# Kernel tuning notes

Measured on AMD Instinct MI355X. Metric: run time of the kernel, lower is better.

The kernel has to match this reference:

```python
import jax, jax.numpy as jnp
import numpy as np

B, T, E, H, L, V = 16, 512, 512, 8, 4, 2048
HS = E // H  # head_size = n_embd // n_head
FF = 4 * E


def _ln(x, g, b):
    m = x.mean(-1, keepdims=True)
    v = ((x - m) ** 2).mean(-1, keepdims=True)
    return (x - m) * jax.lax.rsqrt(v + 1e-5) * g + b


def setup_inputs() -> dict:
    key = jax.random.key(0)
    ks = jax.random.split(key, 16)
    s = jnp.float32(0.02)
    return {
        "idx": jax.random.randint(ks[0], (B, T), 0, V),
        "tok_emb": jax.random.normal(ks[1], (V, E), jnp.float32) * s,
        "pos_emb": jax.random.normal(ks[2], (T, E), jnp.float32) * s,
        "Wq": jax.random.normal(ks[3], (L, E, E), jnp.float32) * s,
        "Wk": jax.random.normal(ks[4], (L, E, E), jnp.float32) * s,
        "Wv": jax.random.normal(ks[5], (L, E, E), jnp.float32) * s,
        "rel": jax.random.normal(ks[6], (L, 2 * T - 1, HS), jnp.float32) * s,
        "Wo": jax.random.normal(ks[7], (L, E, E), jnp.float32) * s,
        "bo": jnp.zeros((L, E), jnp.float32),
        "ln1_g": jnp.ones((L, E), jnp.float32),
        "ln1_b": jnp.zeros((L, E), jnp.float32),
        "W1": jax.random.normal(ks[8], (L, E, FF), jnp.float32) * s,
        "b1": jnp.zeros((L, FF), jnp.float32),
        "W2": jax.random.normal(ks[9], (L, FF, E), jnp.float32) * s,
        "b2": jnp.zeros((L, E), jnp.float32),
        "ln2_g": jnp.ones((L, E), jnp.float32),
        "ln2_b": jnp.zeros((L, E), jnp.float32),
        "lnf_g": jnp.ones((E,), jnp.float32),
        "lnf_b": jnp.zeros((E,), jnp.float32),
        "Wlm": jax.random.normal(ks[10], (E, V), jnp.float32) * s,
        "blm": jnp.zeros((V,), jnp.float32),
    }


def reference(idx, tok_emb, pos_emb, Wq, Wk, Wv, rel, Wo, bo, ln1_g, ln1_b,
              W1, b1, W2, b2, ln2_g, ln2_b, lnf_g, lnf_b, Wlm, blm):
    x = tok_emb[idx] + pos_emb[None, :T]  # (B,T,E)
    ri = jnp.arange(T)
    rel_idx = ri[:, None] - ri[None, :] + (T - 1)  # block_size == T
    causal = ri[:, None] >= ri[None, :]            # (T,T) lower-triangular
    scale = jnp.float32(1.0 / np.sqrt(HS))
    for l in range(L):
        h = _ln(x, ln1_g[l], ln1_b[l])
        # NOTE: torch code does .view(B, H, T, HS) on a (B, T, H*HS) tensor
        # (NOT a transpose) -- jnp.reshape matches row-major view semantics.
        q = (h @ Wq[l]).reshape(B, H, T, HS)
        k = (h @ Wk[l]).reshape(B, H, T, HS)
        v = (h @ Wv[l]).reshape(B, H, T, HS)
        re = rel[l][rel_idx]  # (T,T,HS)
        # rel scores: sum_d q[b,h,i,d]*re[i,j,d]; avoid the 5D intermediate
        scores = jnp.einsum('bhid,bhjd->bhij', q, k) * scale \
               + jnp.einsum('bhid,ijd->bhij', q, re)
        scores = jnp.where(causal, scores, -jnp.inf)
        att = jax.nn.softmax(scores, axis=-1)  # dropout disabled (eval)
        ctx = jnp.einsum('bhij,bhjd->bhid', att, v)
        ctx = jnp.swapaxes(ctx, 1, 2).reshape(B, T, H * HS)
        x = x + ctx @ Wo[l] + bo[l]
        h2 = _ln(x, ln2_g[l], ln2_b[l])
        x = x + jax.nn.relu(h2 @ W1[l] + b1[l]) @ W2[l] + b2[l]
    x = _ln(x, lnf_g, lnf_b)
    return x @ Wlm + blm  # logits (B,T,V)
```

## Files before the change

### kernel.cpp

```cpp
#include <hip/hip_runtime.h>
#include <hip/hip_bf16.h>
#include <stdint.h>

typedef __hip_bfloat16 bf16;
typedef __attribute__((ext_vector_type(8))) short bf16x8;
typedef __attribute__((ext_vector_type(8))) short short8;
typedef __attribute__((ext_vector_type(4))) float f32x4;

#define DEV __device__ __forceinline__

static constexpr int Bn = 16, Tn = 512, En = 512, Hn = 8, Ln = 4, Vn = 2048;
static constexpr int HSn = 64, FFn = 2048, Mn = Bn * Tn;
static constexpr int SQ = 1536;

DEV f32x4 mfma16(bf16x8 a, bf16x8 b, f32x4 c) {
  return __builtin_amdgcn_mfma_f32_16x16x32_bf16(a, b, c, 0, 0, 0);
}
DEV float b2f(bf16 x) { return __bfloat162float(x); }
DEV bf16 f2b(float x) { return __float2bfloat16(x); }
DEV short f2s(float x) { bf16 h = f2b(x); return reinterpret_cast<short&>(h); }
DEV float s2f(short x) { return __bfloat162float(reinterpret_cast<bf16&>(x)); }

DEV void gload16(const void* g, void* l) {
  __builtin_amdgcn_global_load_lds(
      (const __attribute__((address_space(1))) void*)(uintptr_t)g,
      (__attribute__((address_space(3))) void*)(uint32_t)(uintptr_t)l, 16, 0, 0);
}

__global__ __launch_bounds__(256) void ktranspose(const float* __restrict__ in,
                                                  bf16* __restrict__ out, int R, int C,
                                                  long in_zs, long out_zs) {
  __shared__ float tile[32][33];
  int z = blockIdx.z;
  const float* inz = in + (size_t)z * in_zs;
  bf16* outz = out + (size_t)z * out_zs;
  int c0 = blockIdx.x * 32, r0 = blockIdx.y * 32;
  for (int k = 0; k < 32; k += 8)
    tile[threadIdx.y + k][threadIdx.x] =
        inz[(size_t)(r0 + threadIdx.y + k) * C + (c0 + threadIdx.x)];
  __syncthreads();
  for (int k = 0; k < 32; k += 8)
    outz[(size_t)(c0 + threadIdx.y + k) * R + (r0 + threadIdx.x)] =
        f2b(tile[threadIdx.x][threadIdx.y + k]);
}

__global__ __launch_bounds__(256) void kcast(const float* __restrict__ in,
                                             bf16* __restrict__ out, int n) {
  int i = blockIdx.x * 256 + threadIdx.x;
  if (i < n) out[i] = f2b(in[i]);
}

__global__ __launch_bounds__(256) void kembed(const int* __restrict__ idx,
                                              const float* __restrict__ tok,
                                              const float* __restrict__ pos,
                                              bf16* __restrict__ x) {
  int i = blockIdx.x * 256 + threadIdx.x;
  int e8 = (i & 63) * 8;
  int bt = i >> 6;
  int t = bt & (Tn - 1);
  const float* tp = tok + (size_t)idx[bt] * En + e8;
  const float* pp = pos + (size_t)t * En + e8;
  f32x4 t0 = *(const f32x4*)tp, t1 = *(const f32x4*)(tp + 4);
  f32x4 p0 = *(const f32x4*)pp, p1 = *(const f32x4*)(pp + 4);
  short8 ov;
  for (int j = 0; j < 4; j++) {
    ov[j] = f2s(t0[j] + p0[j]);
    ov[j + 4] = f2s(t1[j] + p1[j]);
  }
  *(short8*)(x + (size_t)bt * En + e8) = ov;
}

__global__ __launch_bounds__(256) void kln(const bf16* __restrict__ x,
                                           const float* __restrict__ g,
                                           const float* __restrict__ b,
                                           bf16* __restrict__ out) {
  int row = blockIdx.x * 4 + (threadIdx.x >> 6);
  int lane = threadIdx.x & 63;
  short8 xv = *(const short8*)(x + (size_t)row * En + lane * 8);
  float v[8], s = 0.f;
  for (int j = 0; j < 8; j++) { v[j] = s2f(xv[j]); s += v[j]; }
  for (int m = 1; m < 64; m <<= 1) s += __shfl_xor(s, m);
  float mean = s * (1.f / En);
  float s2 = 0.f;
  for (int j = 0; j < 8; j++) { float d = v[j] - mean; s2 += d * d; }
  for (int m = 1; m < 64; m <<= 1) s2 += __shfl_xor(s2, m);
  float rstd = rsqrtf(s2 * (1.f / En) + 1e-5f);
  f32x4 g0 = *(const f32x4*)(g + lane * 8), g1 = *(const f32x4*)(g + lane * 8 + 4);
  f32x4 b0 = *(const f32x4*)(b + lane * 8), b1 = *(const f32x4*)(b + lane * 8 + 4);
  short8 ov;
  for (int j = 0; j < 4; j++) {
    ov[j] = f2s((v[j] - mean) * rstd * g0[j] + b0[j]);
    ov[j + 4] = f2s((v[j + 4] - mean) * rstd * g1[j] + b1[j]);
  }
  *(short8*)(out + (size_t)row * En + lane * 8) = ov;
}

template <int BM, int BN, int TW, int DB, int SWZ, int NBIAS, int RELU, int MODE>
__global__ __launch_bounds__(TW) void kgemm(const bf16* __restrict__ A,
                                            const bf16* __restrict__ Bt,
                                            const float* __restrict__ bias,
                                            float* __restrict__ outf,
                                            bf16* __restrict__ outh, int Ndim, int K) {
  constexpr int NW = TW / 64;
  constexpr int WCN = NW / 2;
  constexpr int WM = BM / 2, WN = BN / WCN, MI = WM / 16, NI = WN / 16;
  constexpr int NB = DB ? 2 : 1;
  __shared__ bf16 As[NB][BM * 64];
  __shared__ bf16 Bs[NB][BN * 64];
  int t = threadIdx.x, lane = t & 63, w = t >> 6;
  int lr = lane & 15, lg = lane >> 4;
  int sx = lr & 7;
  int wr = w / WCN, wc = w % WCN;
  int bx, by;
  if (SWZ) {
    int id = blockIdx.x + gridDim.x * blockIdx.y;
    int xcd = id & 7, s = id >> 3;
    int gx = gridDim.x;
    by = xcd * 8 + s / gx;
    bx = s % gx;
  } else {
    bx = blockIdx.x; by = blockIdx.y;
  }
  int br = by * BM, bc = bx * BN;
  f32x4 acc[MI][NI] = {};
  int rl = lane >> 3, cb = (lane & 7) ^ rl;
  const bf16* Abase = A + (size_t)(br + w * (BM / NW) + rl) * K + cb * 8;
  const bf16* Bbase = Bt + (size_t)(bc + w * (BN / NW) + rl) * K + cb * 8;

  auto STAGE = [&](int buf, int kt) {
    for (int c = 0; c < BM / (8 * NW); c++)
      gload16(Abase + (size_t)(c * 8) * K + kt, &As[buf][(w * (BM / NW) + c * 8) * 64]);
    for (int c = 0; c < BN / (8 * NW); c++)
      gload16(Bbase + (size_t)(c * 8) * K + kt, &Bs[buf][(w * (BN / NW) + c * 8) * 64]);
  };
  auto COMPUTE = [&](int buf) {
    for (int kk = 0; kk < 2; kk++) {
      int gb = (kk * 4 + lg) ^ sx;
      bf16x8 af[MI], bfr[NI];
      for (int mi = 0; mi < MI; mi++)
        af[mi] = *(const bf16x8*)&As[buf][(wr * WM + mi * 16 + lr) * 64 + gb * 8];
      for (int ni = 0; ni < NI; ni++)
        bfr[ni] = *(const bf16x8*)&Bs[buf][(wc * WN + ni * 16 + lr) * 64 + gb * 8];
      for (int mi = 0; mi < MI; mi++)
        for (int ni = 0; ni < NI; ni++)
          acc[mi][ni] = mfma16(af[mi], bfr[ni], acc[mi][ni]);
    }
  };

  if (DB) {
    STAGE(0, 0);
    __syncthreads();
    int nt = K / 64;
    for (int t2 = 0; t2 < nt; t2++) {
      int cur = t2 & 1;
      if (t2 + 1 < nt) STAGE(cur ^ 1, (t2 + 1) * 64);
      COMPUTE(cur);
      __syncthreads();
    }
  } else {
    for (int kt = 0; kt < K; kt += 64) {
      __syncthreads();
      STAGE(0, kt);
      __syncthreads();
      COMPUTE(0);
    }
  }

  for (int mi = 0; mi < MI; mi++)
    for (int ni = 0; ni < NI; ni++)
      for (int r = 0; r < 4; r++) {
        int row = br + wr * WM + mi * 16 + lg * 4 + r;
        int col = bc + wc * WN + ni * 16 + lr;
        float val = acc[mi][ni][r];
        if (NBIAS) val += bias[col];
        if (RELU) val = fmaxf(val, 0.f);
        if (MODE == 1) {
          bf16* p = outh + (size_t)row * Ndim + col;
          *p = f2b(b2f(*p) + val);
        } else if (MODE == 2) {
          outf[(size_t)row * Ndim + col] = val;
        } else {
          outh[(size_t)row * Ndim + col] = f2b(val);
        }
      }
}

template <int NBIAS, int RELU, int MODE>
__global__ __launch_bounds__(512) void kgemm8(const bf16* __restrict__ A,
                                              const bf16* __restrict__ Bt,
                                              const float* __restrict__ bias,
                                              float* __restrict__ outf,
                                              bf16* __restrict__ outh, int Ndim, int K) {
  __shared__ bf16 As[2][256 * 64];
  __shared__ bf16 Bs[2][256 * 64];
  int t = threadIdx.x, lane = t & 63, w = t >> 6;
  int lr = lane & 15, lg = lane >> 4;
  int sx = lr & 7;
  int wr = w >> 2, wc = w & 3;
  int rl8 = lane >> 3, cb = (lane & 7) ^ rl8;
  int id = blockIdx.x + gridDim.x * blockIdx.y;
  int xcd = id & 7, s = id >> 3;
  int by = xcd * 4 + (s >> 3), bx = s & 7;
  int br = by * 256, bc = bx * 256;
  f32x4 acc[8][4] = {};
  const bf16* Abase = A + (size_t)(br + w * 16 + rl8) * K + cb * 8;
  const bf16* Bbase = Bt + (size_t)(bc + w * 16 + rl8) * K + cb * 8;

  auto STAGEH = [&](int hh, int buf, int kt) {
    int half = hh & 1;
    if (hh < 2) {
      const bf16* g = Abase + (size_t)(half * 128) * K + kt;
      bf16* l = &As[buf][(half * 128 + w * 16) * 64];
      gload16(g, l);
      gload16(g + (size_t)8 * K, l + 8 * 64);
    } else {
      const bf16* g = Bbase + (size_t)(half * 128) * K + kt;
      bf16* l = &Bs[buf][(half * 128 + w * 16) * 64];
      gload16(g, l);
      gload16(g + (size_t)8 * K, l + 8 * 64);
    }
  };

#define PHASE8(Q, P)                                                          \
  do {                                                                        \
    constexpr int mh = (Q) >> 1, nh = (Q) & 1;                                \
    bf16x8 af[4][2], bfr[2][2];                                               \
    _Pragma("unroll") for (int kk = 0; kk < 2; kk++) {                        \
      int gb = (kk * 4 + lg) ^ sx;                                            \
      _Pragma("unroll") for (int i = 0; i < 4; i++)                           \
        af[i][kk] = *(const bf16x8*)&As[P][(wr * 128 + (mh * 4 + i) * 16 + lr) * 64 + gb * 8]; \
      _Pragma("unroll") for (int j = 0; j < 2; j++)                           \
        bfr[j][kk] = *(const bf16x8*)&Bs[P][(wc * 64 + (nh * 2 + j) * 16 + lr) * 64 + gb * 8]; \
    }                                                                         \
    __builtin_amdgcn_s_setprio(1);                                            \
    _Pragma("unroll") for (int i = 0; i < 4; i++)                             \
      _Pragma("unroll") for (int j = 0; j < 2; j++) {                         \
        acc[mh * 4 + i][nh * 2 + j] =                                         \
            mfma16(af[i][0], bfr[j][0], acc[mh * 4 + i][nh * 2 + j]);         \
        acc[mh * 4 + i][nh * 2 + j] =                                         \
            mfma16(af[i][1], bfr[j][1], acc[mh * 4 + i][nh * 2 + j]);         \
      }                                                                       \
    __builtin_amdgcn_s_setprio(0);                                            \
  } while (0)

  int nt = K / 64;
  for (int hh = 0; hh < 4; hh++) STAGEH(hh, 0, 0);
  STAGEH(0, 1, 64);
  STAGEH(1, 1, 64);
  asm volatile("s_waitcnt vmcnt(4)" ::: "memory");
  asm volatile("s_barrier" ::: "memory");
  for (int t2 = 0; t2 < nt; t2++) {
    int p = t2 & 1;
    if (t2 + 1 < nt) STAGEH(2, p ^ 1, (t2 + 1) * 64);
    PHASE8(0, p);
    if (t2 + 1 < nt) STAGEH(3, p ^ 1, (t2 + 1) * 64);
    PHASE8(1, p);
    PHASE8(2, p);
    PHASE8(3, p);
    asm volatile("s_barrier" ::: "memory");
    if (t2 + 2 < nt) {
      STAGEH(0, p, (t2 + 2) * 64);
      STAGEH(1, p, (t2 + 2) * 64);
      asm volatile("s_waitcnt vmcnt(4)" ::: "memory");
      asm volatile("s_barrier" ::: "memory");
    } else if (t2 + 1 < nt) {
      asm volatile("s_waitcnt vmcnt(0)" ::: "memory");
      asm volatile("s_barrier" ::: "memory");
    }
  }
#undef PHASE8
#pragma unroll
  for (int mi = 0; mi < 8; mi++)
#pragma unroll
    for (int ni = 0; ni < 4; ni++)
#pragma unroll
      for (int r = 0; r < 4; r++) {
        int row = br + wr * 128 + mi * 16 + lg * 4 + r;
        int col = bc + wc * 64 + ni * 16 + lr;
        float val = acc[mi][ni][r];
        if (NBIAS) val += bias[col];
        if (RELU) val = fmaxf(val, 0.f);
        if (MODE == 2) outf[(size_t)row * Ndim + col] = val;
        else outh[(size_t)row * Ndim + col] = f2b(val);
      }
}

__global__ __launch_bounds__(512) void kattn(const bf16* __restrict__ qkv,
                                             const bf16* __restrict__ rel,
                                             bf16* __restrict__ ctx) {
  __shared__ bf16 Ks[128 * 64];
  __shared__ bf16 Vs[64 * 128];
  __shared__ bf16 Prel[8][16 * 81];
  __shared__ bf16 Ps[8][16 * 64];
  int pairp = blockIdx.x, bh = blockIdx.y;
  int b = bh >> 3, hh = bh & 7;
  int t = threadIdx.x, lane = t & 63, w = t >> 6;
  int wl = w & 3, wg = w >> 2;
  int lr = lane & 15, lg = lane >> 4;
  int sx = lr & 7;
  int rl8 = lane >> 3, cbk = (lane & 7) ^ rl8;
  const size_t headrow = (size_t)(b * Tn + hh * 64);
  bf16* prw = &Prel[w][0];
  bf16* psw = &Ps[w][0];
  int jp = t >> 3, db = (t & 7) * 8;

  int ia = pairp, ib = 7 - pairp;
  int myblk = wg ? ia : ib;
  int mylast = myblk * 64;
  int i0w = myblk * 64 + wl * 16;
  bf16x8 aq[2];
  {
    int t2 = i0w + lr;
    const bf16* qp = qkv + (headrow + (t2 >> 3)) * SQ + (t2 & 7) * 64;
    aq[0] = *(const bf16x8*)(qp + lg * 8);
    aq[1] = *(const bf16x8*)(qp + 32 + lg * 8);
  }
  f32x4 o[4] = {};
  float m_run = -3e38f, l_run = 0.f;
  int ntiles = (ib >> 1) + 1;

  auto SUBTILE = [&](int jb, bool diag, int su) {
    int njmax = diag ? wl : 3;
    int nmmin = diag ? 3 - wl : 0;
    __builtin_amdgcn_s_setprio(1);
    f32x4 sqk[4] = {};
    for (int nj = 0; nj <= njmax; nj++) {
      int row = su * 64 + nj * 16 + lr;
      bf16x8 kb0 = *(const bf16x8*)&Ks[row * 64 + ((lg ^ sx) * 8)];
      bf16x8 kb1 = *(const bf16x8*)&Ks[row * 64 + (((4 + lg) ^ sx) * 8)];
      sqk[nj] = mfma16(kb0, aq[0], sqk[nj]);
      sqk[nj] = mfma16(kb1, aq[1], sqk[nj]);
    }
    int base = i0w - jb + 448;
    for (int nm = nmmin; nm < 5; nm++) {
      int mrow = base + nm * 16 + lr;
      if (mrow > 1022) mrow = 1022;
      const bf16* rp = rel + (size_t)mrow * 64;
      f32x4 sr = {};
      sr = mfma16(aq[0], *(const bf16x8*)(rp + lg * 8), sr);
      sr = mfma16(aq[1], *(const bf16x8*)(rp + 32 + lg * 8), sr);
      for (int r = 0; r < 4; r++)
        prw[(lg * 4 + r) * 81 + nm * 16 + lr] = f2b(sr[r]);
    }
    __builtin_amdgcn_s_setprio(0);
    float sv[4][4];
    for (int nj = 0; nj < 4; nj++)
      for (int r = 0; r < 4; r++) sv[nj][r] = -3e38f;
    float mloc = -3e38f;
    for (int nj = 0; nj <= njmax; nj++)
      for (int r = 0; r < 4; r++) {
        int jj = nj * 16 + lg * 4 + r;
        float val = sqk[nj][r] * 0.125f + b2f(prw[lr * 81 + (lr - jj + 63)]);
        if (jb + jj > i0w + lr) val = -3e38f;
        sv[nj][r] = val;
        mloc = fmaxf(mloc, val);
      }
    mloc = fmaxf(mloc, __shfl_xor(mloc, 16));
    mloc = fmaxf(mloc, __shfl_xor(mloc, 32));
    float mnew = fmaxf(m_run, mloc);
    float corr = __expf(m_run - mnew);
    m_run = mnew;
    float lsum = 0.f;
    for (int nj = 0; nj < 4; nj++)
      for (int r = 0; r < 4; r++) {
        float p = __expf(sv[nj][r] - mnew);
        lsum += p;
        psw[lr * 64 + (((nj * 2 + (lg >> 1)) ^ sx) * 8) + (lg & 1) * 4 + r] = f2b(p);
      }
    lsum += __shfl_xor(lsum, 16);
    lsum += __shfl_xor(lsum, 32);
    l_run = l_run * corr + lsum;
    for (int r = 0; r < 4; r++) {
      float c = __shfl(corr, lg * 4 + r);
      for (int nd = 0; nd < 4; nd++) o[nd][r] *= c;
    }
    __builtin_amdgcn_s_setprio(1);
    bf16x8 ap0 = *(const bf16x8*)&psw[lr * 64 + ((lg ^ sx) * 8)];
    bf16x8 ap1 = *(const bf16x8*)&psw[lr * 64 + (((4 + lg) ^ sx) * 8)];
    for (int nd = 0; nd < 4; nd++) {
      int d = nd * 16 + lr;
      bf16x8 vb0 = *(const bf16x8*)&Vs[d * 128 + ((su * 8 + (lg ^ sx)) * 8)];
      bf16x8 vb1 = *(const bf16x8*)&Vs[d * 128 + ((su * 8 + ((4 + lg) ^ sx)) * 8)];
      o[nd] = mfma16(ap0, vb0, o[nd]);
      o[nd] = mfma16(ap1, vb1, o[nd]);
    }
    __builtin_amdgcn_s_setprio(0);
  };

  for (int jt = 0; jt < ntiles; jt++) {
    int jbase = jt * 128;
    bf16x8 vv[2];
#pragma unroll
    for (int u = 0; u < 2; u++) {
      int j0 = jbase + jp * 2 + u;
      vv[u] = *(const bf16x8*)(qkv + (headrow + (j0 >> 3)) * SQ + (j0 & 7) * 64 + 1024 + db);
    }
    __syncthreads();
#pragma unroll
    for (int c = 0; c < 2; c++) {
      int row = w * 16 + c * 8 + rl8;
      const bf16* src = qkv + (headrow + ((jbase + row) >> 3)) * SQ +
                        (row & 7) * 64 + 512 + cbk * 8;
      gload16(src, &Ks[(w * 16 + c * 8) * 64]);
    }
    {
      const short* pa = (const short*)&vv[0];
      const short* pb = (const short*)&vv[1];
      int j0 = jp * 2;
      int jblk = j0 >> 3, jin = j0 & 7;
#pragma unroll
      for (int u = 0; u < 8; u++) {
        int d = db + u;
        int idx = d * 128 + ((jblk ^ (d & 7)) * 8) + jin;
        uint32_t pk = (uint32_t)(uint16_t)pa[u] | ((uint32_t)(uint16_t)pb[u] << 16);
        *(uint32_t*)((short*)Vs + idx) = pk;
      }
    }
    __syncthreads();
#pragma unroll
    for (int su = 0; su < 2; su++) {
      int jb = jbase + su * 64;
      if (jb > ib * 64) break;
      if (jb <= mylast) SUBTILE(jb, jb == mylast, su);
    }
  }
  for (int r = 0; r < 4; r++) {
    float linv = 1.f / __shfl(l_run, lg * 4 + r);
    int row = i0w + lg * 4 + r;
    for (int nd = 0; nd < 4; nd++)
      ctx[((size_t)b * Tn + row) * En + hh * 64 + nd * 16 + lr] = f2b(o[nd][r] * linv);
  }
}

extern "C" void kernel_launch(void* const* d_in, const int* in_sizes, int n_in,
                              void* d_out, int out_size, void* d_ws, size_t ws_size,
                              hipStream_t stream) {
  (void)in_sizes; (void)n_in; (void)out_size; (void)ws_size;
  const int* idx = (const int*)d_in[0];
  const float* tok = (const float*)d_in[1];
  const float* pos = (const float*)d_in[2];
  const float* Wq = (const float*)d_in[3];
  const float* Wk = (const float*)d_in[4];
  const float* Wv = (const float*)d_in[5];
  const float* rel = (const float*)d_in[6];
  const float* Wo = (const float*)d_in[7];
  const float* bo = (const float*)d_in[8];
  const float* ln1_g = (const float*)d_in[9];
  const float* ln1_b = (const float*)d_in[10];
  const float* W1 = (const float*)d_in[11];
  const float* b1 = (const float*)d_in[12];
  const float* W2 = (const float*)d_in[13];
  const float* b2 = (const float*)d_in[14];
  const float* ln2_g = (const float*)d_in[15];
  const float* ln2_b = (const float*)d_in[16];
  const float* lnf_g = (const float*)d_in[17];
  const float* lnf_b = (const float*)d_in[18];
  const float* Wlm = (const float*)d_in[19];
  const float* blm = (const float*)d_in[20];

  char* ws = (char*)d_ws;
  bf16* x = (bf16*)(ws + 0);
  bf16* h = (bf16*)(ws + 16777216);
  bf16* qkv = (bf16*)(ws + 25165824);
  bf16* ctx = (bf16*)(ws + 50331648);
  bf16* ffn1 = qkv;
  bf16* wqkvT = (bf16*)(ws + 58720256);
  bf16* woT = wqkvT + (size_t)Ln * SQ * En;
  bf16* w1T = woT + (size_t)Ln * En * En;
  bf16* w2T = w1T + (size_t)Ln * En * FFn;
  bf16* wlmT = w2T + (size_t)Ln * FFn * En;
  bf16* relc = wlmT + (size_t)En * Vn;
  float* outf = (float*)d_out;

  dim3 tb(32, 8);
  ktranspose<<<dim3(16, 16, Ln), tb, 0, stream>>>(Wq, wqkvT, En, En, (long)En * En, (long)SQ * En);
  ktranspose<<<dim3(16, 16, Ln), tb, 0, stream>>>(Wk, wqkvT + 512 * 512, En, En, (long)En * En, (long)SQ * En);
  ktranspose<<<dim3(16, 16, Ln), tb, 0, stream>>>(Wv, wqkvT + 2 * 512 * 512, En, En, (long)En * En, (long)SQ * En);
  ktranspose<<<dim3(16, 16, Ln), tb, 0, stream>>>(Wo, woT, En, En, (long)En * En, (long)En * En);
  ktranspose<<<dim3(64, 16, Ln), tb, 0, stream>>>(W1, w1T, En, FFn, (long)En * FFn, (long)En * FFn);
  ktranspose<<<dim3(16, 64, Ln), tb, 0, stream>>>(W2, w2T, FFn, En, (long)FFn * En, (long)FFn * En);
  ktranspose<<<dim3(64, 16, 1), tb, 0, stream>>>(Wlm, wlmT, En, Vn, 0, 0);
  kcast<<<(Ln * (2 * Tn - 1) * HSn + 255) / 256, 256, 0, stream>>>(
      rel, relc, Ln * (2 * Tn - 1) * HSn);

  kembed<<<(Mn * En / 8) / 256, 256, 0, stream>>>(idx, tok, pos, x);

  for (int l = 0; l < Ln; l++) {
    kln<<<Mn / 4, 256, 0, stream>>>(x, ln1_g + (size_t)l * En, ln1_b + (size_t)l * En, h);
    kgemm<128, 128, 256, 0, 1, 0, 0, 0><<<dim3(12, 64), 256, 0, stream>>>(
        h, wqkvT + (size_t)l * SQ * En, nullptr, nullptr, qkv, SQ, En);
    kattn<<<dim3(4, 128), 512, 0, stream>>>(
        qkv, relc + (size_t)l * (2 * Tn - 1) * HSn, ctx);
    kgemm<128, 128, 512, 1, 1, 1, 0, 1><<<dim3(4, 64), 512, 0, stream>>>(
        ctx, woT + (size_t)l * En * En, bo + (size_t)l * En, nullptr, x, En, En);
    kln<<<Mn / 4, 256, 0, stream>>>(x, ln2_g + (size_t)l * En, ln2_b + (size_t)l * En, h);
    kgemm8<1, 1, 0><<<dim3(8, 32), 512, 0, stream>>>(
        h, w1T + (size_t)l * En * FFn, b1 + (size_t)l * FFn, nullptr, ffn1, FFn, En);
    kgemm<128, 128, 512, 1, 1, 1, 0, 1><<<dim3(4, 64), 512, 0, stream>>>(
        ffn1, w2T + (size_t)l * FFn * En, b2 + (size_t)l * En, nullptr, x, En, FFn);
  }
  kln<<<Mn / 4, 256, 0, stream>>>(x, lnf_g, lnf_b, h);
  kgemm8<1, 0, 2><<<dim3(8, 32), 512, 0, stream>>>(
      h, wlmT, blm, outf, nullptr, Vn, En);
}
```

Before: 611.5 us.

## Merge prep kernels into one launch and use 256x64 kgemm8 for N=512 GEMMs

Fuses the seven weight-transpose launches, the rel cast and the embedding into one kprep kernel that dispatches on block id, removing several launch gaps. Templates kgemm8 on the B-tile width and adds a 256x64 variant with residual-add output, then uses it for the Wo and W2 projections in place of the 128x128 kgemm. The new variant uses a lighter B staging path and a different pipeline schedule. It trades A-tile reuse per block for a different grid shape of 256 blocks with 8-way XCD-aware mapping.

```diff
diff --git a/kernel.cpp b/kernel.cpp
--- a/kernel.cpp
+++ b/kernel.cpp
@@ -27,47 +27,87 @@
       (__attribute__((address_space(3))) void*)(uint32_t)(uintptr_t)l, 16, 0, 0);
 }
 
-__global__ __launch_bounds__(256) void ktranspose(const float* __restrict__ in,
-                                                  bf16* __restrict__ out, int R, int C,
-                                                  long in_zs, long out_zs) {
-  __shared__ float tile[32][33];
-  int z = blockIdx.z;
-  const float* inz = in + (size_t)z * in_zs;
-  bf16* outz = out + (size_t)z * out_zs;
-  int c0 = blockIdx.x * 32, r0 = blockIdx.y * 32;
-  for (int k = 0; k < 32; k += 8)
-    tile[threadIdx.y + k][threadIdx.x] =
-        inz[(size_t)(r0 + threadIdx.y + k) * C + (c0 + threadIdx.x)];
-  __syncthreads();
-  for (int k = 0; k < 32; k += 8)
-    outz[(size_t)(c0 + threadIdx.y + k) * R + (r0 + threadIdx.x)] =
-        f2b(tile[threadIdx.x][threadIdx.y + k]);
-}
-
-__global__ __launch_bounds__(256) void kcast(const float* __restrict__ in,
-                                             bf16* __restrict__ out, int n) {
-  int i = blockIdx.x * 256 + threadIdx.x;
-  if (i < n) out[i] = f2b(in[i]);
-}
-
-__global__ __launch_bounds__(256) void kembed(const int* __restrict__ idx,
-                                              const float* __restrict__ tok,
-                                              const float* __restrict__ pos,
-                                              bf16* __restrict__ x) {
-  int i = blockIdx.x * 256 + threadIdx.x;
-  int e8 = (i & 63) * 8;
-  int bt = i >> 6;
-  int t = bt & (Tn - 1);
-  const float* tp = tok + (size_t)idx[bt] * En + e8;
-  const float* pp = pos + (size_t)t * En + e8;
-  f32x4 t0 = *(const f32x4*)tp, t1 = *(const f32x4*)(tp + 4);
-  f32x4 p0 = *(const f32x4*)pp, p1 = *(const f32x4*)(pp + 4);
-  short8 ov;
-  for (int j = 0; j < 4; j++) {
-    ov[j] = f2s(t0[j] + p0[j]);
-    ov[j + 4] = f2s(t1[j] + p1[j]);
-  }
-  *(short8*)(x + (size_t)bt * En + e8) = ov;
+__global__ __launch_bounds__(256) void kprep(
+    const float* __restrict__ Wq, const float* __restrict__ Wk,
+    const float* __restrict__ Wv, const float* __restrict__ Wo,
+    const float* __restrict__ W1, const float* __restrict__ W2,
+    const float* __restrict__ Wlm, const float* __restrict__ rel,
+    const int* __restrict__ idx, const float* __restrict__ tok,
+    const float* __restrict__ pos,
+    bf16* __restrict__ wqkvT, bf16* __restrict__ woT, bf16* __restrict__ w1T,
+    bf16* __restrict__ w2T, bf16* __restrict__ wlmT, bf16* __restrict__ relc,
+    bf16* __restrict__ x) {
+  int id = blockIdx.x;
+  if (id < 13312) {
+    const float* in;
+    bf16* out;
+    int R, C, z, cx, cy;
+    long in_zs, out_zs;
+    if (id < 3072) {
+      int part = id >> 10, inner = id & 1023;
+      z = inner >> 8;
+      int tile = inner & 255;
+      cx = tile & 15; cy = tile >> 4;
+      in = part == 0 ? Wq : (part == 1 ? Wk : Wv);
+      out = wqkvT + part * 512 * 512;
+      R = En; C = En; in_zs = (long)En * En; out_zs = (long)SQ * En;
+    } else if (id < 4096) {
+      int inner = id - 3072;
+      z = inner >> 8;
+      int tile = inner & 255;
+      cx = tile & 15; cy = tile >> 4;
+      in = Wo; out = woT; R = En; C = En;
+      in_zs = (long)En * En; out_zs = (long)En * En;
+    } else if (id < 8192) {
+      int inner = id - 4096;
+      z = inner >> 10;
+      int tile = inner & 1023;
+      cx = tile & 63; cy = tile >> 6;
+      in = W1; out = w1T; R = En; C = FFn;
+      in_zs = (long)En * FFn; out_zs = (long)En * FFn;
+    } else if (id < 12288) {
+      int inner = id - 8192;
+      z = inner >> 10;
+      int tile = inner & 1023;
+      cx = tile & 15; cy = tile >> 4;
+      in = W2; out = w2T; R = FFn; C = En;
+      in_zs = (long)FFn * En; out_zs = (long)FFn * En;
+    } else {
+      int tile = id - 12288;
+      z = 0;
+      cx = tile & 63; cy = tile >> 6;
+      in = Wlm; out = wlmT; R = En; C = Vn;
+      in_zs = 0; out_zs = 0;
+    }
+    __shared__ float tile_s[32][33];
+    int tx = threadIdx.x & 31, ty = threadIdx.x >> 5;
+    const float* inz = in + (size_t)z * in_zs;
+    bf16* outz = out + (size_t)z * out_zs;
+    int c0 = cx * 32, r0 = cy * 32;
+    for (int k = 0; k < 32; k += 8)
+      tile_s[ty + k][tx] = inz[(size_t)(r0 + ty + k) * C + (c0 + tx)];
+    __syncthreads();
+    for (int k = 0; k < 32; k += 8)
+      outz[(size_t)(c0 + ty + k) * R + (r0 + tx)] = f2b(tile_s[tx][ty + k]);
+  } else if (id < 14335) {
+    int i = (id - 13312) * 256 + threadIdx.x;
+    relc[i] = f2b(rel[i]);
+  } else {
+    int i = (id - 14335) * 256 + threadIdx.x;
+    int e8 = (i & 63) * 8;
+    int bt = i >> 6;
+    int t = bt & (Tn - 1);
+    const float* tp = tok + (size_t)idx[bt] * En + e8;
+    const float* pp = pos + (size_t)t * En + e8;
+    f32x4 t0 = *(const f32x4*)tp, t1 = *(const f32x4*)(tp + 4);
+    f32x4 p0 = *(const f32x4*)pp, p1 = *(const f32x4*)(pp + 4);
+    short8 ov;
+    for (int j = 0; j < 4; j++) {
+      ov[j] = f2s(t0[j] + p0[j]);
+      ov[j + 4] = f2s(t1[j] + p1[j]);
+    }
+    *(short8*)(x + (size_t)bt * En + e8) = ov;
+  }
 }
 
 __global__ __launch_bounds__(256) void kln(const bf16* __restrict__ x,
@@ -185,14 +225,16 @@
       }
 }
 
-template <int NBIAS, int RELU, int MODE>
+template <int BN, int NBIAS, int RELU, int MODE>
 __global__ __launch_bounds__(512) void kgemm8(const bf16* __restrict__ A,
                                               const bf16* __restrict__ Bt,
                                               const float* __restrict__ bias,
                                               float* __restrict__ outf,
                                               bf16* __restrict__ outh, int Ndim, int K) {
+  constexpr int NI = BN / 64;
+  constexpr int BROW = (BN == 256) ? 16 : 8;
   __shared__ bf16 As[2][256 * 64];
-  __shared__ bf16 Bs[2][256 * 64];
+  __shared__ bf16 Bs[2][BN * 64];
   int t = threadIdx.x, lane = t & 63, w = t >> 6;
   int lr = lane & 15, lg = lane >> 4;
   int sx = lr & 7;
@@ -201,87 +243,117 @@
   int id = blockIdx.x + gridDim.x * blockIdx.y;
   int xcd = id & 7, s = id >> 3;
   int by = xcd * 4 + (s >> 3), bx = s & 7;
-  int br = by * 256, bc = bx * 256;
-  f32x4 acc[8][4] = {};
+  int br = by * 256, bc = bx * BN;
+  f32x4 acc[8][NI] = {};
   const bf16* Abase = A + (size_t)(br + w * 16 + rl8) * K + cb * 8;
-  const bf16* Bbase = Bt + (size_t)(bc + w * 16 + rl8) * K + cb * 8;
+  const bf16* Bbase = Bt + (size_t)(bc + w * BROW + rl8) * K + cb * 8;
 
   auto STAGEH = [&](int hh, int buf, int kt) {
-    int half = hh & 1;
     if (hh < 2) {
-      const bf16* g = Abase + (size_t)(half * 128) * K + kt;
-      bf16* l = &As[buf][(half * 128 + w * 16) * 64];
+      const bf16* g = Abase + (size_t)(hh * 128) * K + kt;
+      bf16* l = &As[buf][(hh * 128 + w * 16) * 64];
       gload16(g, l);
       gload16(g + (size_t)8 * K, l + 8 * 64);
-    } else {
+    } else if (BN == 256) {
+      int half = hh & 1;
       const bf16* g = Bbase + (size_t)(half * 128) * K + kt;
       bf16* l = &Bs[buf][(half * 128 + w * 16) * 64];
       gload16(g, l);
       gload16(g + (size_t)8 * K, l + 8 * 64);
+    } else {
+      gload16(Bbase + kt, &Bs[buf][(w * 8) * 64]);
     }
   };
 
-#define PHASE8(Q, P)                                                          \
+#define PH8(MH, NH, NTI, P)                                                   \
   do {                                                                        \
-    constexpr int mh = (Q) >> 1, nh = (Q) & 1;                                \
-    bf16x8 af[4][2], bfr[2][2];                                               \
+    bf16x8 af[4][2], bfr[NTI][2];                                             \
     _Pragma("unroll") for (int kk = 0; kk < 2; kk++) {                        \
       int gb = (kk * 4 + lg) ^ sx;                                            \
       _Pragma("unroll") for (int i = 0; i < 4; i++)                           \
-        af[i][kk] = *(const bf16x8*)&As[P][(wr * 128 + (mh * 4 + i) * 16 + lr) * 64 + gb * 8]; \
-      _Pragma("unroll") for (int j = 0; j < 2; j++)                           \
-        bfr[j][kk] = *(const bf16x8*)&Bs[P][(wc * 64 + (nh * 2 + j) * 16 + lr) * 64 + gb * 8]; \
+        af[i][kk] = *(const bf16x8*)&As[P][(wr * 128 + ((MH) * 4 + i) * 16 + lr) * 64 + gb * 8]; \
+      _Pragma("unroll") for (int j = 0; j < NTI; j++)                         \
+        bfr[j][kk] = *(const bf16x8*)&Bs[P][(wc * (BN / 4) + ((NH) * 2 + j) * 16 + lr) * 64 + gb * 8]; \
     }                                                                         \
     __builtin_amdgcn_s_setprio(1);                                            \
     _Pragma("unroll") for (int i = 0; i < 4; i++)                             \
-      _Pragma("unroll") for (int j = 0; j < 2; j++) {                         \
-        acc[mh * 4 + i][nh * 2 + j] =                                         \
-            mfma16(af[i][0], bfr[j][0], acc[mh * 4 + i][nh * 2 + j]);         \
-        acc[mh * 4 + i][nh * 2 + j] =                                         \
-            mfma16(af[i][1], bfr[j][1], acc[mh * 4 + i][nh * 2 + j]);         \
+      _Pragma("unroll") for (int j = 0; j < NTI; j++) {                       \
+        acc[(MH) * 4 + i][(NH) * 2 + j] =                                     \
+            mfma16(af[i][0], bfr[j][0], acc[(MH) * 4 + i][(NH) * 2 + j]);     \
+        acc[(MH) * 4 + i][(NH) * 2 + j] =                                     \
+            mfma16(af[i][1], bfr[j][1], acc[(MH) * 4 + i][(NH) * 2 + j]);     \
       }                                                                       \
     __builtin_amdgcn_s_setprio(0);                                            \
   } while (0)
 
   int nt = K / 64;
-  for (int hh = 0; hh < 4; hh++) STAGEH(hh, 0, 0);
-  STAGEH(0, 1, 64);
-  STAGEH(1, 1, 64);
-  asm volatile("s_waitcnt vmcnt(4)" ::: "memory");
-  asm volatile("s_barrier" ::: "memory");
-  for (int t2 = 0; t2 < nt; t2++) {
-    int p = t2 & 1;
-    if (t2 + 1 < nt) STAGEH(2, p ^ 1, (t2 + 1) * 64);
-    PHASE8(0, p);
-    if (t2 + 1 < nt) STAGEH(3, p ^ 1, (t2 + 1) * 64);
-    PHASE8(1, p);
-    PHASE8(2, p);
-    PHASE8(3, p);
+  if (BN == 256) {
+    for (int hh = 0; hh < 4; hh++) STAGEH(hh, 0, 0);
+    STAGEH(0, 1, 64);
+    STAGEH(1, 1, 64);
+    asm volatile("s_waitcnt vmcnt(4)" ::: "memory");
     asm volatile("s_barrier" ::: "memory");
-    if (t2 + 2 < nt) {
-      STAGEH(0, p, (t2 + 2) * 64);
-      STAGEH(1, p, (t2 + 2) * 64);
-      asm volatile("s_waitcnt vmcnt(4)" ::: "memory");
+    for (int t2 = 0; t2 < nt; t2++) {
+      int p = t2 & 1;
+      if (t2 + 1 < nt) STAGEH(2, p ^ 1, (t2 + 1) * 64);
+      PH8(0, 0, 2, p);
+      if (t2 + 1 < nt) STAGEH(3, p ^ 1, (t2 + 1) * 64);
+      PH8(0, 1, 2, p);
+      PH8(1, 0, 2, p);
+      PH8(1, 1, 2, p);
       asm volatile("s_barrier" ::: "memory");
-    } else if (t2 + 1 < nt) {
-      asm volatile("s_waitcnt vmcnt(0)" ::: "memory");
+      if (t2 + 2 < nt) {
+        STAGEH(0, p, (t2 + 2) * 64);
+        STAGEH(1, p, (t2 + 2) * 64);
+        asm volatile("s_waitcnt vmcnt(4)" ::: "memory");
+        asm volatile("s_barrier" ::: "memory");
+      } else if (t2 + 1 < nt) {
+        asm volatile("s_waitcnt vmcnt(0)" ::: "memory");
+        asm volatile("s_barrier" ::: "memory");
+      }
+    }
+  } else {
+    STAGEH(0, 0, 0); STAGEH(1, 0, 0); STAGEH(2, 0, 0);
+    STAGEH(0, 1, 64); STAGEH(1, 1, 64);
+    asm volatile("s_waitcnt vmcnt(4)" ::: "memory");
+    asm volatile("s_barrier" ::: "memory");
+    for (int t2 = 0; t2 < nt; t2++) {
+      int p = t2 & 1;
+      if (t2 + 1 < nt) STAGEH(2, p ^ 1, (t2 + 1) * 64);
+      PH8(0, 0, 1, p);
+      PH8(1, 0, 1, p);
       asm volatile("s_barrier" ::: "memory");
-    }
-  }
-#undef PHASE8
+      if (t2 + 2 < nt) {
+        STAGEH(0, p, (t2 + 2) * 64);
+        STAGEH(1, p, (t2 + 2) * 64);
+        asm volatile("s_waitcnt vmcnt(4)" ::: "memory");
+        asm volatile("s_barrier" ::: "memory");
+      } else if (t2 + 1 < nt) {
+        asm volatile("s_waitcnt vmcnt(0)" ::: "memory");
+        asm volatile("s_barrier" ::: "memory");
+      }
+    }
+  }
+#undef PH8
 #pragma unroll
   for (int mi = 0; mi < 8; mi++)
 #pragma unroll
-    for (int ni = 0; ni < 4; ni++)
+    for (int ni = 0; ni < NI; ni++)
 #pragma unroll
       for (int r = 0; r < 4; r++) {
         int row = br + wr * 128 + mi * 16 + lg * 4 + r;
-        int col = bc + wc * 64 + ni * 16 + lr;
+        int col = bc + wc * (BN / 4) + ni * 16 + lr;
         float val = acc[mi][ni][r];
         if (NBIAS) val += bias[col];
         if (RELU) val = fmaxf(val, 0.f);
-        if (MODE == 2) outf[(size_t)row * Ndim + col] = val;
-        else outh[(size_t)row * Ndim + col] = f2b(val);
+        if (MODE == 1) {
+          bf16* p = outh + (size_t)row * Ndim + col;
+          *p = f2b(b2f(*p) + val);
+        } else if (MODE == 2) {
+          outf[(size_t)row * Ndim + col] = val;
+        } else {
+          outh[(size_t)row * Ndim + col] = f2b(val);
+        }
       }
 }
 
@@ -472,18 +544,8 @@
   bf16* relc = wlmT + (size_t)En * Vn;
   float* outf = (float*)d_out;
 
-  dim3 tb(32, 8);
-  ktranspose<<<dim3(16, 16, Ln), tb, 0, stream>>>(Wq, wqkvT, En, En, (long)En * En, (long)SQ * En);
-  ktranspose<<<dim3(16, 16, Ln), tb, 0, stream>>>(Wk, wqkvT + 512 * 512, En, En, (long)En * En, (long)SQ * En);
-  ktranspose<<<dim3(16, 16, Ln), tb, 0, stream>>>(Wv, wqkvT + 2 * 512 * 512, En, En, (long)En * En, (long)SQ * En);
-  ktranspose<<<dim3(16, 16, Ln), tb, 0, stream>>>(Wo, woT, En, En, (long)En * En, (long)En * En);
-  ktranspose<<<dim3(64, 16, Ln), tb, 0, stream>>>(W1, w1T, En, FFn, (long)En * FFn, (long)En * FFn);
-  ktranspose<<<dim3(16, 64, Ln), tb, 0, stream>>>(W2, w2T, FFn, En, (long)FFn * En, (long)FFn * En);
-  ktranspose<<<dim3(64, 16, 1), tb, 0, stream>>>(Wlm, wlmT, En, Vn, 0, 0);
-  kcast<<<(Ln * (2 * Tn - 1) * HSn + 255) / 256, 256, 0, stream>>>(
-      rel, relc, Ln * (2 * Tn - 1) * HSn);
-
-  kembed<<<(Mn * En / 8) / 256, 256, 0, stream>>>(idx, tok, pos, x);
+  kprep<<<16383, 256, 0, stream>>>(Wq, Wk, Wv, Wo, W1, W2, Wlm, rel, idx, tok, pos,
+                                   wqkvT, woT, w1T, w2T, wlmT, relc, x);
 
   for (int l = 0; l < Ln; l++) {
     kln<<<Mn / 4, 256, 0, stream>>>(x, ln1_g + (size_t)l * En, ln1_b + (size_t)l * En, h);
@@ -491,15 +553,15 @@
         h, wqkvT + (size_t)l * SQ * En, nullptr, nullptr, qkv, SQ, En);
     kattn<<<dim3(4, 128), 512, 0, stream>>>(
         qkv, relc + (size_t)l * (2 * Tn - 1) * HSn, ctx);
-    kgemm<128, 128, 512, 1, 1, 1, 0, 1><<<dim3(4, 64), 512, 0, stream>>>(
+    kgemm8<64, 1, 0, 1><<<dim3(8, 32), 512, 0, stream>>>(
         ctx, woT + (size_t)l * En * En, bo + (size_t)l * En, nullptr, x, En, En);
     kln<<<Mn / 4, 256, 0, stream>>>(x, ln2_g + (size_t)l * En, ln2_b + (size_t)l * En, h);
-    kgemm8<1, 1, 0><<<dim3(8, 32), 512, 0, stream>>>(
+    kgemm8<256, 1, 1, 0><<<dim3(8, 32), 512, 0, stream>>>(
         h, w1T + (size_t)l * En * FFn, b1 + (size_t)l * FFn, nullptr, ffn1, FFn, En);
-    kgemm<128, 128, 512, 1, 1, 1, 0, 1><<<dim3(4, 64), 512, 0, stream>>>(
+    kgemm8<64, 1, 0, 1><<<dim3(8, 32), 512, 0, stream>>>(
         ffn1, w2T + (size_t)l * FFn * En, b2 + (size_t)l * En, nullptr, x, En, FFn);
   }
   kln<<<Mn / 4, 256, 0, stream>>>(x, lnf_g, lnf_b, h);
-  kgemm8<1, 0, 2><<<dim3(8, 32), 512, 0, stream>>>(
+  kgemm8<256, 1, 0, 2><<<dim3(8, 32), 512, 0, stream>>>(
       h, wlmT, blm, outf, nullptr, Vn, En);
 }
```

Result: no change. 623.7 us (+2.0%).
